# Optimization experiments

Measured on AMD Instinct MI355X. Metric: run time of the kernel, lower is better.

## Reference

```python
import jax, jax.numpy as jnp
import numpy as np

HEADS = 8
DIM_HEAD = 64
EPS = 1e-5  # fp32 eps in ChanLayerNorm


def chan_layer_norm(x, g):
    # x: [b, c, h, w]; normalize over channel dim with biased variance
    mean = jnp.mean(x, axis=1, keepdims=True)
    var = jnp.var(x, axis=1, keepdims=True)
    return (x - mean) * jax.lax.rsqrt(var + EPS) * g[None, :, None, None]


def setup_inputs() -> dict:
    key = jax.random.key(0)
    k1, k2, k3 = jax.random.split(key, 3)
    dim, inner = 512, HEADS * DIM_HEAD
    fmap = jax.random.normal(k1, (16, dim, 64, 64), dtype=jnp.float32)
    # 1x1 conv weights (no bias); scaled like typical init to keep softmax unsaturated
    w_qkv = jax.random.normal(k2, (3 * inner, dim), dtype=jnp.float32) * 0.02
    w_out = jax.random.normal(k3, (dim, inner), dtype=jnp.float32) * 0.02
    g1 = jnp.ones((dim,), dtype=jnp.float32)
    g2 = jnp.ones((dim,), dtype=jnp.float32)
    return {"fmap": fmap, "g1": g1, "w_qkv": w_qkv, "w_out": w_out, "g2": g2}


def reference(fmap, g1, w_qkv, w_out, g2):
    b, c, X, Y = fmap.shape
    h, dh = HEADS, DIM_HEAD
    n = X * Y  # seq_len
    scale = dh ** -0.5

    x = chan_layer_norm(fmap, g1)
    # 1x1 conv == channel matmul: [b, 3*inner, X, Y]
    qkv = jnp.einsum('bcxy,oc->boxy', x, w_qkv)
    q, k, v = jnp.split(qkv, 3, axis=1)

    def to_bhnc(t):
        # b (h c) x y -> b h n c
        return t.reshape(b, h, dh, n).transpose(0, 1, 3, 2)

    q, k, v = map(to_bhnc, (q, k, v))

    q = jax.nn.softmax(q, axis=-1) * scale          # softmax over feature dim
    k = jax.nn.softmax(k, axis=2)                   # softmax over seq dim
    v = v / jnp.linalg.norm(v, axis=-1, keepdims=True)  # l2norm
    inv_sqrt_n = 1.0 / np.sqrt(n)
    k = k * inv_sqrt_n
    v = v * inv_sqrt_n

    context = jnp.einsum('bhnd,bhne->bhde', k, v)   # small d x e context
    out = jnp.einsum('bhnd,bhde->bhne', q, context)  # [b, h, n, dh]

    # b h n d -> b (h d) x y
    out = out.transpose(0, 1, 3, 2).reshape(b, h * dh, X, Y)
    out = jax.nn.gelu(out, approximate=False)
    out = jnp.einsum('bcxy,oc->boxy', out, w_out)
    return chan_layer_norm(out, g2)
```

## Files before the change

### kernel.cpp

```cpp
#include <hip/hip_runtime.h>

typedef unsigned short u16;
typedef __attribute__((ext_vector_type(2))) float f32x2;
typedef __attribute__((ext_vector_type(4))) float f32x4;
typedef __attribute__((ext_vector_type(8))) short s16x8;
typedef __attribute__((ext_vector_type(8))) u16 u16x8;
typedef __attribute__((ext_vector_type(4))) u16 u16x4;

#define NB 16
#define CD 512
#define NS 4096
#define NHD 8

#define SBAR  __builtin_amdgcn_s_barrier()
#define SCHED __builtin_amdgcn_sched_barrier(0)
#define LGKM0 asm volatile("s_waitcnt lgkmcnt(0)" ::: "memory")
#define PRIO1 __builtin_amdgcn_s_setprio(1)
#define PRIO0 __builtin_amdgcn_s_setprio(0)

__device__ __forceinline__ float bf2f(u16 u){
  union { unsigned int i; float f; } z; z.i = ((unsigned int)u) << 16; return z.f;
}
__device__ __forceinline__ u16 f2bf(float f){
  union { float f; unsigned int i; } z; z.f = f;
  unsigned int i = z.i;
  return (u16)((i + 0x7fffu + ((i >> 16) & 1u)) >> 16);
}
__device__ __forceinline__ float gelu_f(float x){
  return 0.5f * x * (1.0f + erff(x * 0.70710678118654752440f));
}
__device__ __forceinline__ void gl_lds16(const u16* g, u16* l){
  __builtin_amdgcn_global_load_lds((const __attribute__((address_space(1))) void*)(g),
                                   (__attribute__((address_space(3))) void*)(l), 16, 0, 0);
}

__global__ void prep_w_k(const float* __restrict__ wqkv, const float* __restrict__ g1,
                         const float* __restrict__ wout, u16* __restrict__ w1b,
                         u16* __restrict__ w2b){
  int i = blockIdx.x * 256 + threadIdx.x;
  if (i < 1536*512) {
    w1b[i] = f2bf(wqkv[i] * g1[i & 511]);
  } else {
    int j = i - 1536*512;
    w2b[j] = f2bf(wout[j]);
  }
}

__global__ __launch_bounds__(512) void ln1t_k(const float* __restrict__ fmap,
                                              u16* __restrict__ xlnT){
  int b = blockIdx.y, n0 = blockIdx.x * 32;
  int t = threadIdx.x;
  int lane = t & 63, wv = t >> 6;
  __shared__ float Lb[512][36];
  __shared__ u16 Tt[64][36];
  __shared__ float red1[8][8][4], red2[8][8][4];
  __shared__ float mean_s[32], rstd_s[32];

  int ng = t & 7;
  float s1[4] = {0,0,0,0}, s2[4] = {0,0,0,0};
  const float* fb = fmap + ((size_t)b*CD)*NS + n0 + ng*4;
  #pragma unroll
  for (int it = 0; it < 8; ++it){
    int q = it*512 + t;
    int c = q >> 3;
    f32x4 v = *(const f32x4*)&fb[(size_t)c*NS];
    *(f32x4*)&Lb[c][ng*4] = v;
    #pragma unroll
    for (int j = 0; j < 4; ++j){ s1[j] += v[j]; s2[j] += v[j]*v[j]; }
  }
  #pragma unroll
  for (int off = 8; off < 64; off <<= 1)
    #pragma unroll
    for (int j = 0; j < 4; ++j){
      s1[j] += __shfl_xor(s1[j], off, 64);
      s2[j] += __shfl_xor(s2[j], off, 64);
    }
  if (lane < 8){
    #pragma unroll
    for (int j = 0; j < 4; ++j){ red1[wv][lane][j] = s1[j]; red2[wv][lane][j] = s2[j]; }
  }
  __syncthreads();
  if (t < 32){
    int g = t >> 2, j = t & 3;
    float a = 0.f, bq = 0.f;
    #pragma unroll
    for (int w = 0; w < 8; ++w){ a += red1[w][g][j]; bq += red2[w][g][j]; }
    float mn = a * (1.f/512.f);
    float var = bq * (1.f/512.f) - mn*mn;
    mean_s[t] = mn; rstd_s[t] = rsqrtf(var + 1e-5f);
  }
  __syncthreads();

  for (int ct = 0; ct < 8; ++ct){
    {
      int cl = t >> 3, n4 = (t & 7) * 4;
      f32x4 v = *(const f32x4*)&Lb[ct*64 + cl][n4];
      u16x4 pk;
      #pragma unroll
      for (int j = 0; j < 4; ++j)
        pk[j] = f2bf((v[j] - mean_s[n4+j]) * rstd_s[n4+j]);
      *(u16x4*)&Tt[cl][n4] = pk;
    }
    __syncthreads();
    {
      int nr = t >> 4, c4 = t & 15;
      u16x4 w;
      #pragma unroll
      for (int j = 0; j < 4; ++j) w[j] = Tt[c4*4 + j][nr];
      *(u16x4*)&xlnT[((size_t)b*NS + n0 + nr)*CD + ct*64 + c4*4] = w;
    }
    __syncthreads();
  }
}

__global__ __launch_bounds__(512, 4) void gemm1_k(const u16* __restrict__ A,
                                                  const u16* __restrict__ Bm,
                                                  u16* __restrict__ Cm){
  __shared__ u16 lds[3][12288];
  int bi = blockIdx.x;
  int xcd = bi & 7, r2 = bi >> 3;
  int oo  = r2 % 12;
  int x   = (r2 / 12) & 15;
  int zl  = r2 / 192;
  int z   = xcd*2 + zl;
  int o0 = oo*128, bn0 = x*256;
  int t = threadIdx.x;
  int lane = t & 63, wv = t >> 6;
  int wm = wv >> 2, wn = wv & 3;
  int fr = lane & 15, fg = lane >> 4;
  const u16* Ab = A + (size_t)o0*512;
  const u16* Bb = Bm + ((size_t)z*NS + bn0)*512;

  int l8  = lane >> 3;
  int c8l = (lane & 7) ^ l8;
  int shf = c8l >> 2;
  int sc  = (c8l & 3) * 8;

  f32x4 acc[4][4];
  #pragma unroll
  for (int i=0;i<4;++i)
    #pragma unroll
    for (int j=0;j<4;++j) acc[i][j] = (f32x4){0.f,0.f,0.f,0.f};
  s16x8 afr[4], bfr[4];

  auto stA = [&](int slot, int kt){
    int L = wv*8 + l8;
    int r = shf*64 + L;
    gl_lds16(Ab + (size_t)r*512 + kt + sc, &lds[slot][wv*512]);
  };
  auto stB = [&](int slot, int kt, int i){
    int L = i*64 + wv*8 + l8;
    int r = shf*128 + L;
    gl_lds16(Bb + (size_t)r*512 + kt + sc, &lds[slot][4096 + i*4096 + wv*512]);
  };
  auto ldA = [&](int slot){
    #pragma unroll
    for (int mi=0;mi<4;++mi){
      int L  = mi*16 + fr;
      int c8 = (wm*4 + fg) ^ (L & 7);
      afr[mi] = *(const s16x8*)&lds[slot][L*64 + c8*8];
    }
  };
  auto ldB = [&](int slot){
    #pragma unroll
    for (int nj=0;nj<4;++nj){
      int L  = (wn&1)*64 + nj*16 + fr;
      int c8 = ((wn>>1)*4 + fg) ^ (L & 7);
      bfr[nj] = *(const s16x8*)&lds[slot][4096 + L*64 + c8*8];
    }
  };

  stA(0,0);  stB(0,0,0);  stB(0,0,1);
  stA(1,32); stB(1,32,0); stB(1,32,1);
  asm volatile("s_waitcnt vmcnt(3)" ::: "memory");
  SBAR; SCHED;

  #pragma unroll
  for (int kt=0; kt<16; ++kt){
    int slot = kt % 3;
    ldA(slot); ldB(slot);
    if (kt < 14){
      int ns = (kt+2)%3, kn = (kt+2)*32;
      stA(ns,kn); stB(ns,kn,0); stB(ns,kn,1);
    }
    LGKM0; SCHED;
    PRIO1;
    #pragma unroll
    for (int mi=0;mi<4;++mi)
      #pragma unroll
      for (int nj=0;nj<4;++nj)
        acc[mi][nj] = __builtin_amdgcn_mfma_f32_16x16x32_bf16(
            afr[mi], bfr[nj], acc[mi][nj], 0,0,0);
    PRIO0;
    if (kt < 14)       asm volatile("s_waitcnt vmcnt(3)" ::: "memory");
    else if (kt == 14) asm volatile("s_waitcnt vmcnt(0)" ::: "memory");
    SBAR; SCHED;
  }

  size_t cb = (size_t)z * 1536 * NS;
  #pragma unroll
  for (int mi=0;mi<4;++mi)
    #pragma unroll
    for (int nj=0;nj<4;++nj){
      int row = o0 + wm*64 + mi*16 + fg*4;
      int col = bn0 + wn*64 + nj*16 + fr;
      #pragma unroll
      for (int r=0;r<4;++r)
        Cm[cb + (size_t)(row+r)*NS + col] = f2bf(acc[mi][nj][r]);
    }
}

__global__ __launch_bounds__(512, 2) void gemm2ln_k(const u16* __restrict__ A,
                                                    const u16* __restrict__ Bm,
                                                    const float* __restrict__ g2,
                                                    float* __restrict__ out){
  __shared__ u16 lds[3][20480];
  int x = blockIdx.x, z = blockIdx.y;
  int n0 = x*128;
  int t = threadIdx.x;
  int lane = t & 63, wv = t >> 6;
  int wm = wv >> 1, wn = wv & 1;
  int fr = lane & 15, fg = lane >> 4;
  const u16* Ab = A;
  const u16* Bb = Bm + ((size_t)z*NS + n0)*512;
  int rA = t >> 2, cx = t & 3;

  f32x4 acc[8][4];
  #pragma unroll
  for (int i=0;i<8;++i)
    #pragma unroll
    for (int j=0;j<4;++j) acc[i][j] = (f32x4){0.f,0.f,0.f,0.f};
  s16x8 afr[4], bfr[4];

  auto swz4 = [](int c, int r){ return (c ^ (r & 3) ^ ((r >> 2) & 3)) & 3; };
  auto stA = [&](int slot, int kt, int bt){
    int r = bt*128 + rA;
    gl_lds16(Ab + (size_t)r*512 + kt + (swz4(cx,r)<<3), &lds[slot][bt*4096 + wv*512]);
  };
  auto stB = [&](int slot, int kt){
    int r = rA;
    gl_lds16(Bb + (size_t)r*512 + kt + (swz4(cx,r)<<3), &lds[slot][16384 + wv*512]);
  };
  auto ldA = [&](int slot, int h){
    #pragma unroll
    for (int mi=0;mi<4;++mi){
      int R = wm*128 + (h*4+mi)*16 + fr;
      afr[mi] = *(const s16x8*)&lds[slot][R*32 + (swz4(fg,R)<<3)];
    }
  };
  auto ldB = [&](int slot){
    #pragma unroll
    for (int nj=0;nj<4;++nj){
      int R = wn*64 + nj*16 + fr;
      bfr[nj] = *(const s16x8*)&lds[slot][16384 + R*32 + (swz4(fg,R)<<3)];
    }
  };
  auto mm16 = [&](int h){
    #pragma unroll
    for (int mi=0;mi<4;++mi)
      #pragma unroll
      for (int nj=0;nj<4;++nj)
        acc[h*4+mi][nj] = __builtin_amdgcn_mfma_f32_16x16x32_bf16(
            afr[mi], bfr[nj], acc[h*4+mi][nj], 0,0,0);
  };

  #pragma unroll
  for (int p=0;p<2;++p){ stA(p,p*32,0); stA(p,p*32,1); stB(p,p*32); stA(p,p*32,2); stA(p,p*32,3); }
  asm volatile("s_waitcnt vmcnt(5)" ::: "memory");
  SBAR; SCHED;

  #pragma unroll
  for (int kt=0; kt<16; ++kt){
    int slot = kt%3, ns = (kt+2)%3, kn = (kt+2)*32;
    ldA(slot,0); ldB(slot);
    if (kt<14){ stA(ns,kn,0); stA(ns,kn,1); stB(ns,kn); }
    SBAR; LGKM0; SCHED;
    PRIO1; mm16(0); PRIO0;
    SBAR; SCHED;
    ldA(slot,1);
    if (kt<14){ stA(ns,kn,2); stA(ns,kn,3); }
    SBAR; LGKM0; SCHED;
    PRIO1; mm16(1); PRIO0;
    if (kt<14)       asm volatile("s_waitcnt vmcnt(5)" ::: "memory");
    else if (kt==14) asm volatile("s_waitcnt vmcnt(0)" ::: "memory");
    SBAR; SCHED;
  }

  __syncthreads();
  float* red1 = (float*)&lds[0][0];
  float* red2 = red1 + 512;
  float* ms   = red2 + 512;
  float* rs   = ms + 128;
  float s1[4], s2[4];
  #pragma unroll
  for (int nj=0;nj<4;++nj){
    float a = 0.f, b2 = 0.f;
    #pragma unroll
    for (int mi=0;mi<8;++mi)
      #pragma unroll
      for (int r=0;r<4;++r){ float v = acc[mi][nj][r]; a += v; b2 += v*v; }
    s1[nj] = a; s2[nj] = b2;
  }
  #pragma unroll
  for (int off=16; off<64; off<<=1)
    #pragma unroll
    for (int nj=0;nj<4;++nj){
      s1[nj] += __shfl_xor(s1[nj], off, 64);
      s2[nj] += __shfl_xor(s2[nj], off, 64);
    }
  if (fg == 0){
    #pragma unroll
    for (int nj=0;nj<4;++nj){
      int c = wn*64 + nj*16 + fr;
      red1[wm*128 + c] = s1[nj];
      red2[wm*128 + c] = s2[nj];
    }
  }
  __syncthreads();
  if (t < 128){
    float a  = red1[t] + red1[128+t] + red1[256+t] + red1[384+t];
    float b2 = red2[t] + red2[128+t] + red2[256+t] + red2[384+t];
    float mn = a * (1.f/512.f);
    float var = b2 * (1.f/512.f) - mn*mn;
    ms[t] = mn; rs[t] = rsqrtf(var + 1e-5f);
  }
  __syncthreads();
  float mc[4], rc[4];
  #pragma unroll
  for (int nj=0;nj<4;++nj){
    int c = wn*64 + nj*16 + fr;
    mc[nj] = ms[c]; rc[nj] = rs[c];
  }
  float* ob = out + (size_t)z*CD*NS + n0;
  #pragma unroll
  for (int mi=0;mi<8;++mi)
    #pragma unroll
    for (int r=0;r<4;++r){
      int row = wm*128 + mi*16 + fg*4 + r;
      float gg = g2[row];
      #pragma unroll
      for (int nj=0;nj<4;++nj)
        ob[(size_t)row*NS + wn*64 + nj*16 + fr] = (acc[mi][nj][r] - mc[nj])*rc[nj]*gg;
    }
}

__global__ __launch_bounds__(256) void ctxpart_k(const u16* __restrict__ qkv,
                                                 float* __restrict__ part,
                                                 float* __restrict__ mS){
  int chunk = blockIdx.x, bh = blockIdx.y;
  int b = bh >> 3, h = bh & 7;
  int t = threadIdx.x;
  int lane = t & 63, wv = t >> 6;
  int fr = lane & 15, fg = lane >> 4;
  __shared__ u16 KT[64*128];
  __shared__ u16 VT[64*128];
  __shared__ float invn_s[128];
  const u16* kb = qkv + ((size_t)(b*1536 + 512  + h*64))*NS;
  const u16* vb = qkv + ((size_t)(b*1536 + 1024 + h*64))*NS;
  int d = t >> 2, q = t & 3;

  float mloc = -3.0e38f;
  #pragma unroll
  for (int nt = 0; nt < 4; ++nt)
    #pragma unroll
    for (int s = 0; s < 4; ++s){
      u16x8 kk = *(const u16x8*)&kb[(size_t)d*NS + chunk*512 + nt*128 + q*32 + s*8];
      #pragma unroll
      for (int j = 0; j < 8; ++j) mloc = fmaxf(mloc, bf2f(kk[j]));
    }
  mloc = fmaxf(mloc, __shfl_xor(mloc, 1, 64));
  mloc = fmaxf(mloc, __shfl_xor(mloc, 2, 64));
  float sloc = 0.f;

  f32x4 acc[4][4];
  #pragma unroll
  for (int i=0;i<4;++i)
    #pragma unroll
    for (int j=0;j<4;++j) acc[i][j] = (f32x4){0.f,0.f,0.f,0.f};

  for (int nt = 0; nt < 4; ++nt){
    int n0 = chunk*512 + nt*128;
    if (nt) __syncthreads();
    u16x8 kreg[4];
    #pragma unroll
    for (int s = 0; s < 4; ++s){
      int c0 = q*32 + s*8;
      u16x8 vv = *(const u16x8*)&vb[(size_t)d*NS + n0 + c0];
      *(u16x8*)&VT[d*128 + (c0 ^ ((d&7)<<3))] = vv;
      kreg[s] = *(const u16x8*)&kb[(size_t)d*NS + n0 + c0];
    }
    __syncthreads();
    if (t < 128){
      float ss = 0.f;
      #pragma unroll
      for (int e = 0; e < 64; ++e){
        float xv = bf2f(VT[e*128 + (t ^ ((e&7)<<3))]);
        ss += xv*xv;
      }
      invn_s[t] = rsqrtf(ss);
    }
    __syncthreads();
    #pragma unroll
    for (int s = 0; s < 4; ++s){
      int c0 = q*32 + s*8;
      u16x8 kk = kreg[s];
      u16x8 ek;
      #pragma unroll
      for (int j = 0; j < 8; ++j){
        float e = __expf(bf2f(kk[j]) - mloc);
        sloc += e;
        ek[j] = f2bf(e * invn_s[c0 + j]);
      }
      *(u16x8*)&KT[d*128 + (c0 ^ ((d&7)<<3))] = ek;
    }
    __syncthreads();
    int kc = wv*32 + fg*8;
    s16x8 af[4], bfr[4];
    #pragma unroll
    for (int i=0;i<4;++i){
      int ra = i*16 + fr;
      af[i]  = *(const s16x8*)&KT[ra*128 + (kc ^ ((ra&7)<<3))];
      bfr[i] = *(const s16x8*)&VT[ra*128 + (kc ^ ((ra&7)<<3))];
    }
    #pragma unroll
    for (int i=0;i<4;++i)
      #pragma unroll
      for (int j=0;j<4;++j)
        acc[i][j] = __builtin_amdgcn_mfma_f32_16x16x32_bf16(af[i], bfr[j], acc[i][j], 0,0,0);
  }

  sloc += __shfl_xor(sloc, 1, 64);
  sloc += __shfl_xor(sloc, 2, 64);
  if (q == 0){
    size_t mb = ((size_t)bh*8 + chunk)*128;
    mS[mb + d]      = mloc;
    mS[mb + 64 + d] = sloc;
  }

  float* buf0 = (float*)KT;
  float* buf1 = (float*)VT;
  auto dump = [&](float* bf){
    #pragma unroll
    for (int i=0;i<4;++i)
      #pragma unroll
      for (int j=0;j<4;++j)
        #pragma unroll
        for (int r=0;r<4;++r) bf[((i*4+j)*4+r)*64 + lane] = acc[i][j][r];
  };
  auto addin = [&](float* bf){
    #pragma unroll
    for (int i=0;i<4;++i)
      #pragma unroll
      for (int j=0;j<4;++j)
        #pragma unroll
        for (int r=0;r<4;++r) acc[i][j][r] += bf[((i*4+j)*4+r)*64 + lane];
  };
  __syncthreads();
  if (wv==1) dump(buf0);
  if (wv==3) dump(buf1);
  __syncthreads();
  if (wv==0) addin(buf0);
  if (wv==2) addin(buf1);
  __syncthreads();
  if (wv==2) dump(buf0);
  __syncthreads();
  if (wv==0){
    addin(buf0);
    float* pp = part + ((size_t)bh*8 + chunk)*4096;
    #pragma unroll
    for (int i=0;i<4;++i)
      #pragma unroll
      for (int j=0;j<4;++j)
        #pragma unroll
        for (int r=0;r<4;++r)
          pp[(i*16+fg*4+r)*64 + j*16+fr] = acc[i][j][r];
  }
}

__global__ void ctxred_k(const float* __restrict__ part, const float* __restrict__ mS,
                         float* __restrict__ ctx){
  int bh = blockIdx.x, t = threadIdx.x;
  __shared__ float fs[8][64];
  if (t < 64){
    int d = t;
    float mc[8];
    float mx = -3.0e38f;
    #pragma unroll
    for (int c=0;c<8;++c){ mc[c] = mS[((size_t)bh*8 + c)*128 + d]; mx = fmaxf(mx, mc[c]); }
    float es[8]; float denom = 0.f;
    #pragma unroll
    for (int c=0;c<8;++c){
      es[c] = __expf(mc[c] - mx);
      denom += es[c] * mS[((size_t)bh*8 + c)*128 + 64 + d];
    }
    float inv = 1.0f / (denom * 4096.0f);
    #pragma unroll
    for (int c=0;c<8;++c) fs[c][d] = es[c] * inv;
  }
  __syncthreads();
  #pragma unroll
  for (int i=0;i<16;++i){
    int idx = t + i*256;
    int d = idx >> 6;
    float s = 0.f;
    #pragma unroll
    for (int ch=0; ch<8; ++ch) s += fs[ch][d] * part[((size_t)bh*8 + ch)*4096 + idx];
    ctx[(size_t)bh*4096 + idx] = s;
  }
}

__global__ __launch_bounds__(256) void attnout_k(const u16* __restrict__ qkv,
                                                 const float* __restrict__ ctx,
                                                 u16* __restrict__ gT){
  int bh = blockIdx.y;
  int b = bh >> 3, h = bh & 7;
  int n0 = blockIdx.x * 256;
  int t = threadIdx.x;
  int lane = t & 63, wv = t >> 6;
  int fr = lane & 15, fg = lane >> 4;
  __shared__ u16 P[256][72];
  __shared__ u16 cT[64][72];

  const float* cs = ctx + (size_t)bh*4096;
  #pragma unroll
  for (int i=0;i<16;++i){
    int idx = i*256 + t;
    int d = idx >> 6, e = idx & 63;
    cT[e][d] = f2bf(cs[idx]);
  }

  const u16* qb = qkv + ((size_t)(b*1536 + h*64))*NS + n0 + t;
  float p[64];
  #pragma unroll
  for (int d=0; d<64; ++d) p[d] = bf2f(qb[(size_t)d*NS]);
  float m = p[0];
  #pragma unroll
  for (int d=1; d<64; ++d) m = fmaxf(m, p[d]);
  float s = 0.f;
  #pragma unroll
  for (int d=0; d<64; ++d){ p[d] = __expf(p[d]-m); s += p[d]; }
  float inv = 0.125f / s;
  #pragma unroll
  for (int d0=0; d0<8; ++d0){
    u16x8 pk;
    #pragma unroll
    for (int j=0;j<8;++j) pk[j] = f2bf(p[d0*8+j] * inv);
    *(u16x8*)&P[t][d0*8] = pk;
  }
  __syncthreads();

  f32x4 acc[4][4];
  #pragma unroll
  for (int i=0;i<4;++i)
    #pragma unroll
    for (int j=0;j<4;++j) acc[i][j] = (f32x4){0.f,0.f,0.f,0.f};
  #pragma unroll
  for (int k=0; k<2; ++k){
    s16x8 af[4], bfr[4];
    #pragma unroll
    for (int i=0;i<4;++i){
      af[i]  = *(const s16x8*)&P[wv*64 + i*16 + fr][k*32 + fg*8];
      bfr[i] = *(const s16x8*)&cT[i*16 + fr][k*32 + fg*8];
    }
    #pragma unroll
    for (int i=0;i<4;++i)
      #pragma unroll
      for (int j=0;j<4;++j)
        acc[i][j] = __builtin_amdgcn_mfma_f32_16x16x32_bf16(af[i], bfr[j], acc[i][j], 0,0,0);
  }

  #pragma unroll
  for (int i=0;i<4;++i)
    #pragma unroll
    for (int j=0;j<4;++j)
      #pragma unroll
      for (int r=0;r<4;++r)
        P[wv*64 + i*16 + fg*4 + r][j*16 + fr] = f2bf(gelu_f(acc[i][j][r]));

  int sub = lane >> 4, e4 = (lane & 15) * 4;
  #pragma unroll
  for (int it=0; it<16; ++it){
    int row = wv*64 + it*4 + sub;
    *(u16x4*)&gT[((size_t)b*NS + n0 + row)*CD + h*64 + e4] = *(u16x4*)&P[row][e4];
  }
}

extern "C" void kernel_launch(void* const* d_in, const int* in_sizes, int n_in,
                              void* d_out, int out_size, void* d_ws, size_t ws_size,
                              hipStream_t stream) {
  const float* fmap = (const float*)d_in[0];
  const float* g1   = (const float*)d_in[1];
  const float* wqkv = (const float*)d_in[2];
  const float* wout = (const float*)d_in[3];
  const float* g2   = (const float*)d_in[4];
  float* out = (float*)d_out;

  char* ws = (char*)d_ws;
  size_t off = 0;
  auto alloc = [&](size_t bytes) -> void* {
    void* p = ws + off;
    off += (bytes + 255) & ~(size_t)255;
    return p;
  };
  u16*   qkv  = (u16*)alloc((size_t)16*1536*4096*2);
  u16*   xlnT = (u16*)alloc((size_t)16*4096*512*2);
  u16*   gT   = xlnT;
  float* part = (float*)alloc((size_t)128*8*4096*4);
  float* mS   = (float*)alloc((size_t)128*8*128*4);
  float* ctx  = (float*)alloc((size_t)128*4096*4);
  u16*   w1b  = (u16*)alloc((size_t)1536*512*2);
  u16*   w2b  = (u16*)alloc((size_t)512*512*2);
  if (off > ws_size) return;

  prep_w_k<<<4096, 256, 0, stream>>>(wqkv, g1, wout, w1b, w2b);
  ln1t_k<<<dim3(128,16), 512, 0, stream>>>(fmap, xlnT);
  gemm1_k<<<3072, 512, 0, stream>>>(w1b, xlnT, qkv);
  ctxpart_k<<<dim3(8,128), 256, 0, stream>>>(qkv, part, mS);
  ctxred_k<<<128, 256, 0, stream>>>(part, mS, ctx);
  attnout_k<<<dim3(16,128), 256, 0, stream>>>(qkv, ctx, gT);
  gemm2ln_k<<<dim3(32,16), 512, 0, stream>>>(w2b, gT, g2, out);
}
```

Before: 336.2 us.

## Deepen gemm1 LDS pipeline to four stages and reswizzle gemm2 tiles

gemm1 moves from a 3-slot to a 4-slot LDS ring, prefetching three k-tiles ahead, and drops the explicit lgkmcnt(0) wait before the MFMAs. gemm2ln switches to a 64-wide row layout with an XOR swizzle matching gemm1, issues all five global-to-LDS loads per k-step at once, and removes the intermediate barriers and lgkm waits between its two MFMA halves. The aim is more memory latency hiding and less barrier stall per iteration. In exchange gemm1 uses more LDS, which may cut occupancy, and the removed barriers rely on the compiler inserting LDS waits and on the slot reuse distance being safe.

After: 354.5 us. 5.5% more time.

```diff
diff --git a/kernel.cpp b/kernel.cpp
--- a/kernel.cpp
+++ b/kernel.cpp
@@ -14,7 +14,6 @@
 
 #define SBAR  __builtin_amdgcn_s_barrier()
 #define SCHED __builtin_amdgcn_sched_barrier(0)
-#define LGKM0 asm volatile("s_waitcnt lgkmcnt(0)" ::: "memory")
 #define PRIO1 __builtin_amdgcn_s_setprio(1)
 #define PRIO0 __builtin_amdgcn_s_setprio(0)
 
@@ -116,7 +115,7 @@
 __global__ __launch_bounds__(512, 4) void gemm1_k(const u16* __restrict__ A,
                                                   const u16* __restrict__ Bm,
                                                   u16* __restrict__ Cm){
-  __shared__ u16 lds[3][12288];
+  __shared__ u16 lds[4][12288];
   int bi = blockIdx.x;
   int xcd = bi & 7, r2 = bi >> 3;
   int oo  = r2 % 12;
@@ -172,18 +171,18 @@
 
   stA(0,0);  stB(0,0,0);  stB(0,0,1);
   stA(1,32); stB(1,32,0); stB(1,32,1);
-  asm volatile("s_waitcnt vmcnt(3)" ::: "memory");
+  stA(2,64); stB(2,64,0); stB(2,64,1);
+  asm volatile("s_waitcnt vmcnt(6)" ::: "memory");
   SBAR; SCHED;
 
   #pragma unroll
   for (int kt=0; kt<16; ++kt){
-    int slot = kt % 3;
+    int slot = kt & 3;
     ldA(slot); ldB(slot);
-    if (kt < 14){
-      int ns = (kt+2)%3, kn = (kt+2)*32;
+    if (kt < 13){
+      int ns = (kt+3) & 3, kn = (kt+3)*32;
       stA(ns,kn); stB(ns,kn,0); stB(ns,kn,1);
     }
-    LGKM0; SCHED;
     PRIO1;
     #pragma unroll
     for (int mi=0;mi<4;++mi)
@@ -192,8 +191,8 @@
         acc[mi][nj] = __builtin_amdgcn_mfma_f32_16x16x32_bf16(
             afr[mi], bfr[nj], acc[mi][nj], 0,0,0);
     PRIO0;
-    if (kt < 14)       asm volatile("s_waitcnt vmcnt(3)" ::: "memory");
-    else if (kt == 14) asm volatile("s_waitcnt vmcnt(0)" ::: "memory");
+    if (kt < 13)       asm volatile("s_waitcnt vmcnt(3)" ::: "memory");
+    else if (kt == 13) asm volatile("s_waitcnt vmcnt(0)" ::: "memory");
     SBAR; SCHED;
   }
 
@@ -223,7 +222,9 @@
   int fr = lane & 15, fg = lane >> 4;
   const u16* Ab = A;
   const u16* Bb = Bm + ((size_t)z*NS + n0)*512;
-  int rA = t >> 2, cx = t & 3;
+
+  int l8  = lane >> 3;
+  int c8d = lane & 7;
 
   f32x4 acc[8][4];
   #pragma unroll
@@ -232,27 +233,36 @@
     for (int j=0;j<4;++j) acc[i][j] = (f32x4){0.f,0.f,0.f,0.f};
   s16x8 afr[4], bfr[4];
 
-  auto swz4 = [](int c, int r){ return (c ^ (r & 3) ^ ((r >> 2) & 3)) & 3; };
   auto stA = [&](int slot, int kt, int bt){
-    int r = bt*128 + rA;
-    gl_lds16(Ab + (size_t)r*512 + kt + (swz4(cx,r)<<3), &lds[slot][bt*4096 + wv*512]);
+    int L  = bt*64 + wv*8 + l8;
+    int q  = c8d ^ (l8 & 7);
+    int r  = (q >> 2)*256 + L;
+    int col = kt + (q & 3)*8;
+    gl_lds16(Ab + (size_t)r*512 + col, &lds[slot][(bt*64 + wv*8)*64]);
   };
   auto stB = [&](int slot, int kt){
-    int r = rA;
-    gl_lds16(Bb + (size_t)r*512 + kt + (swz4(cx,r)<<3), &lds[slot][16384 + wv*512]);
+    int L  = wv*8 + l8;
+    int q  = c8d ^ (l8 & 7);
+    int r  = (q >> 2)*64 + L;
+    int col = kt + (q & 3)*8;
+    gl_lds16(Bb + (size_t)r*512 + col, &lds[slot][16384 + (wv*8)*64]);
   };
   auto ldA = [&](int slot, int h){
     #pragma unroll
     for (int mi=0;mi<4;++mi){
       int R = wm*128 + (h*4+mi)*16 + fr;
-      afr[mi] = *(const s16x8*)&lds[slot][R*32 + (swz4(fg,R)<<3)];
+      int L = R & 255, half = R >> 8;
+      int c8 = (half*4 + fg) ^ (L & 7);
+      afr[mi] = *(const s16x8*)&lds[slot][L*64 + c8*8];
     }
   };
   auto ldB = [&](int slot){
     #pragma unroll
     for (int nj=0;nj<4;++nj){
       int R = wn*64 + nj*16 + fr;
-      bfr[nj] = *(const s16x8*)&lds[slot][16384 + R*32 + (swz4(fg,R)<<3)];
+      int L = R & 63, half = R >> 6;
+      int c8 = (half*4 + fg) ^ (L & 7);
+      bfr[nj] = *(const s16x8*)&lds[slot][16384 + L*64 + c8*8];
     }
   };
   auto mm16 = [&](int h){
@@ -271,15 +281,14 @@
 
   #pragma unroll
   for (int kt=0; kt<16; ++kt){
-    int slot = kt%3, ns = (kt+2)%3, kn = (kt+2)*32;
+    int slot = kt%3;
     ldA(slot,0); ldB(slot);
-    if (kt<14){ stA(ns,kn,0); stA(ns,kn,1); stB(ns,kn); }
-    SBAR; LGKM0; SCHED;
+    if (kt<14){
+      int ns = (kt+2)%3, kn = (kt+2)*32;
+      stA(ns,kn,0); stA(ns,kn,1); stB(ns,kn); stA(ns,kn,2); stA(ns,kn,3);
+    }
     PRIO1; mm16(0); PRIO0;
-    SBAR; SCHED;
     ldA(slot,1);
-    if (kt<14){ stA(ns,kn,2); stA(ns,kn,3); }
-    SBAR; LGKM0; SCHED;
     PRIO1; mm16(1); PRIO0;
     if (kt<14)       asm volatile("s_waitcnt vmcnt(5)" ::: "memory");
     else if (kt==14) asm volatile("s_waitcnt vmcnt(0)" ::: "memory");
```
